# Kernel optimization log

Hardware: AMD Instinct MI355X
Metric: run time of the kernel (lower is better)

The kernel has to match this reference:

```python
import jax, jax.numpy as jnp
import numpy as np

EMBED_DIM = 1024
NUM_HEADS = 16
HEAD_DIM = EMBED_DIM // NUM_HEADS


def setup_inputs() -> dict:
    key = jax.random.key(0)
    ks = jax.random.split(key, 6)
    B, S, D = 4, 2048, EMBED_DIM
    std = 1.0 / np.sqrt(D)
    x = jax.random.normal(ks[0], (B, S, D), dtype=jnp.float32)
    wq = jax.random.normal(ks[1], (D, D), dtype=jnp.float32) * std
    wk = jax.random.normal(ks[2], (D, D), dtype=jnp.float32) * std
    wv = jax.random.normal(ks[3], (D, D), dtype=jnp.float32) * std
    wo = jax.random.normal(ks[4], (D, D), dtype=jnp.float32) * std
    bo = jax.random.normal(ks[5], (D,), dtype=jnp.float32) * 0.01
    return {"x": x, "wq": wq, "wk": wk, "wv": wv, "wo": wo, "bo": bo}


def reference(x, wq, wk, wv, wo, bo):
    B, S, D = x.shape
    H, Hd = NUM_HEADS, HEAD_DIM
    scale = 1.0 / jnp.sqrt(jnp.asarray(Hd, x.dtype))
    # nn.Linear computes x @ W.T; split into heads -> [B, H, S, Hd]
    q = (x @ wq.T).reshape(B, S, H, Hd).transpose(0, 2, 1, 3)
    k = (x @ wk.T).reshape(B, S, H, Hd).transpose(0, 2, 1, 3)
    v = (x @ wv.T).reshape(B, S, H, Hd).transpose(0, 2, 1, 3)
    scores = jnp.einsum("bhqd,bhkd->bhqk", q, k) * scale  # [B,H,S,S]
    attn = jax.nn.softmax(scores, axis=-1)
    ctx = jnp.einsum("bhqk,bhkd->bhqd", attn, v)
    ctx = ctx.transpose(0, 2, 1, 3).reshape(B, S, D)
    return ctx @ wo.T + bo
```

## Files before the change

### kernel.cpp

```cpp
#include <hip/hip_runtime.h>

typedef __bf16 bf16x8 __attribute__((ext_vector_type(8)));
typedef float f32x4 __attribute__((ext_vector_type(4)));
typedef unsigned u32x4 __attribute__((ext_vector_type(4)));
typedef unsigned short u16;

#define GAS __attribute__((address_space(1)))
#define LAS __attribute__((address_space(3)))

static __device__ __forceinline__ void gload16(const void* g, void* l) {
  __builtin_amdgcn_global_load_lds((const GAS unsigned int*)g, (LAS unsigned int*)l, 16, 0, 0);
}

static __device__ __forceinline__ u16 f2bf(float f) {
  unsigned u = __builtin_bit_cast(unsigned, f);
  u += 0x7fffu + ((u >> 16) & 1u);
  return (u16)(u >> 16);
}

static __device__ __forceinline__ unsigned pk2(float lo, float hi) {
  ushort2 u;
  u.x = __builtin_bit_cast(u16, (__bf16)lo);
  u.y = __builtin_bit_cast(u16, (__bf16)hi);
  return __builtin_bit_cast(unsigned, u);
}

__global__ void cvt_kernel(const float* __restrict__ src, u16* __restrict__ dst, int n4) {
  int i = blockIdx.x * 256 + threadIdx.x;
  if (i >= n4) return;
  float4 v = reinterpret_cast<const float4*>(src)[i];
  ushort4 o;
  o.x = f2bf(v.x); o.y = f2bf(v.y); o.z = f2bf(v.z); o.w = f2bf(v.w);
  reinterpret_cast<ushort4*>(dst)[i] = o;
}

__global__ void cvt_w_kernel(const float* __restrict__ w0, const float* __restrict__ w1,
                             const float* __restrict__ w2, const float* __restrict__ w3,
                             u16* __restrict__ d0, u16* __restrict__ d1,
                             u16* __restrict__ d2, u16* __restrict__ d3) {
  int sel = blockIdx.x >> 10;
  int i = (blockIdx.x & 1023) * 256 + threadIdx.x;
  const float* s = sel == 0 ? w0 : sel == 1 ? w1 : sel == 2 ? w2 : w3;
  u16* d = sel == 0 ? d0 : sel == 1 ? d1 : sel == 2 ? d2 : d3;
  float4 v = reinterpret_cast<const float4*>(s)[i];
  ushort4 o;
  o.x = f2bf(v.x); o.y = f2bf(v.y); o.z = f2bf(v.z); o.w = f2bf(v.w);
  reinterpret_cast<ushort4*>(d)[i] = o;
}

__global__ void gemm_qkv(const u16* __restrict__ A, const u16* __restrict__ W,
                         u16* __restrict__ Qo, u16* __restrict__ Ko, u16* __restrict__ Vo) {
  __shared__ u16 As[128 * 32];
  __shared__ u16 Bs[128 * 32];
  const int t = threadIdx.x;
  const int lane = t & 63;
  const int w = t >> 6;
  const int wr = w >> 1, wc = w & 1;
  const int l15 = lane & 15, lhi = lane >> 4;
  const int swz = (blockIdx.x & 7) * 192 + (blockIdx.x >> 3);
  const int bm = swz / 24, bn = swz % 24;

  f32x4 acc[4][4];
#pragma unroll
  for (int a = 0; a < 4; ++a)
#pragma unroll
    for (int b = 0; b < 4; ++b) acc[a][b] = (f32x4){0.f, 0.f, 0.f, 0.f};

  const u16* ag = A + (size_t)(bm * 128 + (t >> 2)) * 1024 + (t & 3) * 8;
  const u16* bg = W + (size_t)(bn * 128 + (t >> 2)) * 1024 + (t & 3) * 8;
  u16* as_p = &As[t * 8];
  u16* bs_p = &Bs[t * 8];

  for (int kt = 0; kt < 32; ++kt) {
    gload16(ag, as_p);
    gload16(ag + 64 * 1024, as_p + 2048);
    gload16(bg, bs_p);
    gload16(bg + 64 * 1024, bs_p + 2048);
    ag += 32; bg += 32;
    __syncthreads();
    bf16x8 af[4], bfr[4];
#pragma unroll
    for (int mt = 0; mt < 4; ++mt)
      af[mt] = *(const bf16x8*)&As[(wr * 64 + mt * 16 + l15) * 32 + lhi * 8];
#pragma unroll
    for (int nt = 0; nt < 4; ++nt)
      bfr[nt] = *(const bf16x8*)&Bs[(wc * 64 + nt * 16 + l15) * 32 + lhi * 8];
#pragma unroll
    for (int mt = 0; mt < 4; ++mt)
#pragma unroll
      for (int nt = 0; nt < 4; ++nt)
        acc[mt][nt] = __builtin_amdgcn_mfma_f32_16x16x32_bf16(af[mt], bfr[nt], acc[mt][nt], 0, 0, 0);
    __syncthreads();
  }

  const int tsel = bn >> 3;
  const int m0 = bm * 128 + wr * 64;
  const int n0 = bn * 128 + wc * 64;
  const int bb = bm >> 4;
  if (tsel == 0) {
    const float qs = 0.125f * 1.4426950408889634f;
#pragma unroll
    for (int nt = 0; nt < 4; ++nt) {
      int n = n0 + nt * 16 + l15;
      int c = n & 1023, h = c >> 6, hd = c & 63;
      size_t base = (size_t)(bb * 16 + h) * 2048 * 64 + hd;
#pragma unroll
      for (int mt = 0; mt < 4; ++mt)
#pragma unroll
        for (int i = 0; i < 4; ++i) {
          int s = (m0 + mt * 16 + lhi * 4 + i) & 2047;
          Qo[base + (size_t)s * 64] = f2bf(acc[mt][nt][i] * qs);
        }
    }
  } else if (tsel == 1) {
#pragma unroll
    for (int nt = 0; nt < 4; ++nt) {
      int n = n0 + nt * 16 + l15;
      int c = n & 1023, h = c >> 6, hd = c & 63;
      size_t base = (size_t)(bb * 16 + h) * 2048 * 64 + hd;
#pragma unroll
      for (int mt = 0; mt < 4; ++mt)
#pragma unroll
        for (int i = 0; i < 4; ++i) {
          int s = (m0 + mt * 16 + lhi * 4 + i) & 2047;
          Ko[base + (size_t)s * 64] = f2bf(acc[mt][nt][i]);
        }
    }
  } else {
#pragma unroll
    for (int nt = 0; nt < 4; ++nt) {
      int n = n0 + nt * 16 + l15;
      int c = n & 1023, h = c >> 6, hd = c & 63;
#pragma unroll
      for (int mt = 0; mt < 4; ++mt) {
        int s0 = (m0 + mt * 16 + lhi * 4) & 2047;
        int sp0 = ((s0 >> 4) & 1) * 4 + ((s0 >> 2) & 3) * 8 + (s0 >> 5) * 32;
        ushort4 pk;
        pk.x = f2bf(acc[mt][nt][0]);
        pk.y = f2bf(acc[mt][nt][1]);
        pk.z = f2bf(acc[mt][nt][2]);
        pk.w = f2bf(acc[mt][nt][3]);
        *(ushort4*)&Vo[((size_t)(bb * 16 + h) * 64 + hd) * 2048 + sp0] = pk;
      }
    }
  }
}

__global__ __launch_bounds__(256, 4) void attn_kernel(const u16* __restrict__ Q,
                                                      const u16* __restrict__ K,
                                                      const u16* __restrict__ Vp,
                                                      u16* __restrict__ Ctx) {
  __shared__ u16 Ks[2 * 64 * 64];
  __shared__ u16 Vs[2 * 64 * 64];
  const int t = threadIdx.x;
  const int lane = t & 63;
  const int w = t >> 6;
  const int l15 = lane & 15, lhi = lane >> 4;
  const int swz = (blockIdx.x & 7) * 128 + (blockIdx.x >> 3);
  const int qt = swz & 15, pair = swz >> 4;
  const u16* qp = Q + (size_t)pair * 2048 * 64;
  const u16* kp = K + (size_t)pair * 2048 * 64;
  const u16* vp = Vp + (size_t)pair * 64 * 2048;

  const int qrA = qt * 128 + w * 32 + l15;
  bf16x8 qfA[2], qfB[2];
  qfA[0] = *(const bf16x8*)&qp[(size_t)qrA * 64 + lhi * 8];
  qfA[1] = *(const bf16x8*)&qp[(size_t)qrA * 64 + 32 + lhi * 8];
  qfB[0] = *(const bf16x8*)&qp[(size_t)(qrA + 16) * 64 + lhi * 8];
  qfB[1] = *(const bf16x8*)&qp[(size_t)(qrA + 16) * 64 + 32 + lhi * 8];

  const u32x4 ow = {0x3F803F80u, 0x3F803F80u, 0x3F803F80u, 0x3F803F80u};
  const bf16x8 onesf = __builtin_bit_cast(bf16x8, ow);

  const int swzq = (l15 & 7) << 3;
  const int kofs0 = l15 * 64 + ((lhi * 8) ^ swzq);
  const int kofs1 = l15 * 64 + ((32 + lhi * 8) ^ swzq);

  f32x4 coA[4], coB[4], laA, laB;
  laA = (f32x4){0.f, 0.f, 0.f, 0.f};
  laB = laA;
#pragma unroll
  for (int n = 0; n < 4; ++n) { coA[n] = laA; coB[n] = laA; }

  auto stage = [&](int cb, int tt) {
#pragma unroll
    for (int j = 0; j < 2; ++j) {
      int c = j * 256 + t;
      int r = c >> 3, c8 = (c & 7) * 8;
      gload16(kp + (size_t)(tt * 64 + r) * 64 + (c8 ^ ((r & 7) << 3)), &Ks[cb + c * 8]);
    }
#pragma unroll
    for (int j = 0; j < 2; ++j) {
      int c = j * 256 + t;
      int r = c >> 3, c8 = (c & 7) * 8;
      gload16(vp + (size_t)r * 2048 + tt * 64 + (c8 ^ ((r & 7) << 3)), &Vs[cb + c * 8]);
    }
  };

  auto softmax_sub = [&](f32x4 (&sa)[4], unsigned (&pw)[4][2]) {
#pragma unroll
    for (int nt = 0; nt < 4; ++nt)
#pragma unroll
      for (int e = 0; e < 4; ++e) sa[nt][e] = __builtin_exp2f(sa[nt][e]);
#pragma unroll
    for (int nt = 0; nt < 4; ++nt) {
      pw[nt][0] = pk2(sa[nt][0], sa[nt][1]);
      pw[nt][1] = pk2(sa[nt][2], sa[nt][3]);
    }
  };

  stage(0, 0);

  for (int kt = 0; kt < 32; ++kt) {
    const int cb = (kt & 1) * 4096;
    if (kt < 31) {
      stage(cb ^ 4096, kt + 1);
      asm volatile("s_waitcnt vmcnt(4)" ::: "memory");
    } else {
      asm volatile("s_waitcnt vmcnt(0)" ::: "memory");
    }
    __builtin_amdgcn_s_barrier();

    f32x4 saA[4], saB[4];
    __builtin_amdgcn_s_setprio(1);
#pragma unroll
    for (int nt = 0; nt < 4; ++nt) {
      bf16x8 kf0 = *(const bf16x8*)&Ks[cb + kofs0 + nt * 1024];
      bf16x8 kf1 = *(const bf16x8*)&Ks[cb + kofs1 + nt * 1024];
      f32x4 zA = (f32x4){0.f, 0.f, 0.f, 0.f};
      f32x4 zB = zA;
      zA = __builtin_amdgcn_mfma_f32_16x16x32_bf16(kf0, qfA[0], zA, 0, 0, 0);
      zB = __builtin_amdgcn_mfma_f32_16x16x32_bf16(kf0, qfB[0], zB, 0, 0, 0);
      saA[nt] = __builtin_amdgcn_mfma_f32_16x16x32_bf16(kf1, qfA[1], zA, 0, 0, 0);
      saB[nt] = __builtin_amdgcn_mfma_f32_16x16x32_bf16(kf1, qfB[1], zB, 0, 0, 0);
    }
    __builtin_amdgcn_s_setprio(0);

    unsigned pwA[4][2], pwB[4][2];
    softmax_sub(saA, pwA);
    softmax_sub(saB, pwB);

    __builtin_amdgcn_s_setprio(1);
#pragma unroll
    for (int ks = 0; ks < 2; ++ks) {
      u32x4 awA = {pwA[2 * ks][0], pwA[2 * ks][1], pwA[2 * ks + 1][0], pwA[2 * ks + 1][1]};
      u32x4 awB = {pwB[2 * ks][0], pwB[2 * ks][1], pwB[2 * ks + 1][0], pwB[2 * ks + 1][1]};
      bf16x8 afA = __builtin_bit_cast(bf16x8, awA);
      bf16x8 afB = __builtin_bit_cast(bf16x8, awB);
      laA = __builtin_amdgcn_mfma_f32_16x16x32_bf16(afA, onesf, laA, 0, 0, 0);
      laB = __builtin_amdgcn_mfma_f32_16x16x32_bf16(afB, onesf, laB, 0, 0, 0);
      const int vo = l15 * 64 + (((ks ? 32 : 0) + lhi * 8) ^ swzq);
#pragma unroll
      for (int nthd = 0; nthd < 4; ++nthd) {
        bf16x8 vf = *(const bf16x8*)&Vs[cb + vo + nthd * 1024];
        coA[nthd] = __builtin_amdgcn_mfma_f32_16x16x32_bf16(afA, vf, coA[nthd], 0, 0, 0);
        coB[nthd] = __builtin_amdgcn_mfma_f32_16x16x32_bf16(afB, vf, coB[nthd], 0, 0, 0);
      }
    }
    __builtin_amdgcn_s_setprio(0);
    __builtin_amdgcn_s_barrier();
  }

  float liA[4], liB[4];
#pragma unroll
  for (int i = 0; i < 4; ++i) {
    liA[i] = 1.0f / laA[i];
    liB[i] = 1.0f / laB[i];
  }
  const int bb = pair >> 4, hh = pair & 15;
  const int sbase = qt * 128 + w * 32 + lhi * 4;
#pragma unroll
  for (int nthd = 0; nthd < 4; ++nthd) {
    int hd = nthd * 16 + l15;
#pragma unroll
    for (int i = 0; i < 4; ++i) {
      Ctx[(size_t)(bb * 2048 + sbase + i) * 1024 + hh * 64 + hd] = f2bf(coA[nthd][i] * liA[i]);
      Ctx[(size_t)(bb * 2048 + sbase + 16 + i) * 1024 + hh * 64 + hd] = f2bf(coB[nthd][i] * liB[i]);
    }
  }
}

__global__ void gemm_out(const u16* __restrict__ A, const u16* __restrict__ W,
                         const float* __restrict__ Bo, float* __restrict__ Out) {
  __shared__ u16 As[128 * 32];
  __shared__ u16 Bs[128 * 32];
  const int t = threadIdx.x;
  const int lane = t & 63;
  const int w = t >> 6;
  const int wr = w >> 1, wc = w & 1;
  const int l15 = lane & 15, lhi = lane >> 4;
  const int swz = (blockIdx.x & 7) * 64 + (blockIdx.x >> 3);
  const int bm = swz >> 3, bn = swz & 7;

  f32x4 acc[4][4];
#pragma unroll
  for (int a = 0; a < 4; ++a)
#pragma unroll
    for (int b = 0; b < 4; ++b) acc[a][b] = (f32x4){0.f, 0.f, 0.f, 0.f};

  const u16* ag = A + (size_t)(bm * 128 + (t >> 2)) * 1024 + (t & 3) * 8;
  const u16* bg = W + (size_t)(bn * 128 + (t >> 2)) * 1024 + (t & 3) * 8;
  u16* as_p = &As[t * 8];
  u16* bs_p = &Bs[t * 8];

  for (int kt = 0; kt < 32; ++kt) {
    gload16(ag, as_p);
    gload16(ag + 64 * 1024, as_p + 2048);
    gload16(bg, bs_p);
    gload16(bg + 64 * 1024, bs_p + 2048);
    ag += 32; bg += 32;
    __syncthreads();
    bf16x8 af[4], bfr[4];
#pragma unroll
    for (int mt = 0; mt < 4; ++mt)
      af[mt] = *(const bf16x8*)&As[(wr * 64 + mt * 16 + l15) * 32 + lhi * 8];
#pragma unroll
    for (int nt = 0; nt < 4; ++nt)
      bfr[nt] = *(const bf16x8*)&Bs[(wc * 64 + nt * 16 + l15) * 32 + lhi * 8];
#pragma unroll
    for (int mt = 0; mt < 4; ++mt)
#pragma unroll
      for (int nt = 0; nt < 4; ++nt)
        acc[mt][nt] = __builtin_amdgcn_mfma_f32_16x16x32_bf16(af[mt], bfr[nt], acc[mt][nt], 0, 0, 0);
    __syncthreads();
  }

  const int m0 = bm * 128 + wr * 64;
  const int n0 = bn * 128 + wc * 64;
#pragma unroll
  for (int nt = 0; nt < 4; ++nt) {
    int n = n0 + nt * 16 + l15;
    float bias = Bo[n];
#pragma unroll
    for (int mt = 0; mt < 4; ++mt)
#pragma unroll
      for (int i = 0; i < 4; ++i) {
        int m = m0 + mt * 16 + lhi * 4 + i;
        Out[(size_t)m * 1024 + n] = acc[mt][nt][i] + bias;
      }
  }
}

extern "C" void kernel_launch(void* const* d_in, const int* in_sizes, int n_in,
                              void* d_out, int out_size, void* d_ws, size_t ws_size,
                              hipStream_t stream) {
  const float* x  = (const float*)d_in[0];
  const float* wq = (const float*)d_in[1];
  const float* wk = (const float*)d_in[2];
  const float* wv = (const float*)d_in[3];
  const float* wo = (const float*)d_in[4];
  const float* bo = (const float*)d_in[5];
  float* out = (float*)d_out;

  u16* xb    = (u16*)d_ws;
  u16* wqkvb = xb + (size_t)8 * 1024 * 1024;
  u16* wob   = wqkvb + (size_t)3 * 1024 * 1024;
  u16* qb    = wob + (size_t)1 * 1024 * 1024;
  u16* kb    = qb + (size_t)8 * 1024 * 1024;
  u16* vtb   = kb + (size_t)8 * 1024 * 1024;
  u16* ctxb  = xb;

  cvt_kernel<<<8192, 256, 0, stream>>>(x, xb, 2097152);
  cvt_w_kernel<<<4096, 256, 0, stream>>>(wq, wk, wv, wo,
                                         wqkvb, wqkvb + 1048576, wqkvb + 2097152, wob);
  gemm_qkv<<<64 * 24, 256, 0, stream>>>(xb, wqkvb, qb, kb, vtb);
  attn_kernel<<<1024, 256, 0, stream>>>(qb, kb, vtb, ctxb);
  gemm_out<<<64 * 8, 256, 0, stream>>>(ctxb, wob, bo, out);
}
```

Before: 216.8 us.

## Double-buffer GEMM LDS tiles, restructure attention prefetch sync, merge conversion kernels

Both GEMM kernels now keep two LDS buffers and issue the next K-tile's global-to-LDS loads before computing on the current one. The aim is to hide global load latency behind MFMA work, and each iteration now needs only one barrier. The attention loop moves its wait and barrier to the end of the iteration, so the prefetch of the next K/V tile overlaps the whole current compute. The two fp32-to-bf16 conversion kernels become a single launch. The cost is doubled LDS per GEMM block, which may reduce occupancy.

Measured after the change: 213.4 us. Within noise of the previous version (-1.6%).

```diff
diff --git a/kernel.cpp b/kernel.cpp
--- a/kernel.cpp
+++ b/kernel.cpp
@@ -25,33 +25,36 @@
   return __builtin_bit_cast(unsigned, u);
 }
 
-__global__ void cvt_kernel(const float* __restrict__ src, u16* __restrict__ dst, int n4) {
+__global__ void cvt_all(const float* __restrict__ x, const float* __restrict__ wq,
+                        const float* __restrict__ wk, const float* __restrict__ wv,
+                        const float* __restrict__ wo, u16* __restrict__ xb,
+                        u16* __restrict__ wqkvb, u16* __restrict__ wob) {
   int i = blockIdx.x * 256 + threadIdx.x;
-  if (i >= n4) return;
-  float4 v = reinterpret_cast<const float4*>(src)[i];
+  float4 v;
+  ushort4* dst;
+  if (i < 2097152) {
+    v = reinterpret_cast<const float4*>(x)[i];
+    dst = reinterpret_cast<ushort4*>(xb) + i;
+  } else if (i < 2883584) {
+    int j = i - 2097152;
+    const float* s = j < 262144 ? wq : (j < 524288 ? wk : wv);
+    int jj = j < 262144 ? j : (j < 524288 ? j - 262144 : j - 524288);
+    v = reinterpret_cast<const float4*>(s)[jj];
+    dst = reinterpret_cast<ushort4*>(wqkvb) + j;
+  } else {
+    int j = i - 2883584;
+    v = reinterpret_cast<const float4*>(wo)[j];
+    dst = reinterpret_cast<ushort4*>(wob) + j;
+  }
   ushort4 o;
   o.x = f2bf(v.x); o.y = f2bf(v.y); o.z = f2bf(v.z); o.w = f2bf(v.w);
-  reinterpret_cast<ushort4*>(dst)[i] = o;
-}
-
-__global__ void cvt_w_kernel(const float* __restrict__ w0, const float* __restrict__ w1,
-                             const float* __restrict__ w2, const float* __restrict__ w3,
-                             u16* __restrict__ d0, u16* __restrict__ d1,
-                             u16* __restrict__ d2, u16* __restrict__ d3) {
-  int sel = blockIdx.x >> 10;
-  int i = (blockIdx.x & 1023) * 256 + threadIdx.x;
-  const float* s = sel == 0 ? w0 : sel == 1 ? w1 : sel == 2 ? w2 : w3;
-  u16* d = sel == 0 ? d0 : sel == 1 ? d1 : sel == 2 ? d2 : d3;
-  float4 v = reinterpret_cast<const float4*>(s)[i];
-  ushort4 o;
-  o.x = f2bf(v.x); o.y = f2bf(v.y); o.z = f2bf(v.z); o.w = f2bf(v.w);
-  reinterpret_cast<ushort4*>(d)[i] = o;
+  *dst = o;
 }
 
 __global__ void gemm_qkv(const u16* __restrict__ A, const u16* __restrict__ W,
                          u16* __restrict__ Qo, u16* __restrict__ Ko, u16* __restrict__ Vo) {
-  __shared__ u16 As[128 * 32];
-  __shared__ u16 Bs[128 * 32];
+  __shared__ u16 As[2 * 128 * 32];
+  __shared__ u16 Bs[2 * 128 * 32];
   const int t = threadIdx.x;
   const int lane = t & 63;
   const int w = t >> 6;
@@ -68,29 +71,35 @@
 
   const u16* ag = A + (size_t)(bm * 128 + (t >> 2)) * 1024 + (t & 3) * 8;
   const u16* bg = W + (size_t)(bn * 128 + (t >> 2)) * 1024 + (t & 3) * 8;
-  u16* as_p = &As[t * 8];
-  u16* bs_p = &Bs[t * 8];
+
+  auto stage = [&](int cb, int kt) {
+    gload16(ag + kt * 32, &As[cb + t * 8]);
+    gload16(ag + kt * 32 + 64 * 1024, &As[cb + t * 8 + 2048]);
+    gload16(bg + kt * 32, &Bs[cb + t * 8]);
+    gload16(bg + kt * 32 + 64 * 1024, &Bs[cb + t * 8 + 2048]);
+  };
+
+  stage(0, 0);
+  asm volatile("s_waitcnt vmcnt(0)" ::: "memory");
+  __builtin_amdgcn_s_barrier();
 
   for (int kt = 0; kt < 32; ++kt) {
-    gload16(ag, as_p);
-    gload16(ag + 64 * 1024, as_p + 2048);
-    gload16(bg, bs_p);
-    gload16(bg + 64 * 1024, bs_p + 2048);
-    ag += 32; bg += 32;
-    __syncthreads();
+    const int cb = (kt & 1) * 4096;
+    if (kt < 31) stage(cb ^ 4096, kt + 1);
     bf16x8 af[4], bfr[4];
 #pragma unroll
     for (int mt = 0; mt < 4; ++mt)
-      af[mt] = *(const bf16x8*)&As[(wr * 64 + mt * 16 + l15) * 32 + lhi * 8];
+      af[mt] = *(const bf16x8*)&As[cb + (wr * 64 + mt * 16 + l15) * 32 + lhi * 8];
 #pragma unroll
     for (int nt = 0; nt < 4; ++nt)
-      bfr[nt] = *(const bf16x8*)&Bs[(wc * 64 + nt * 16 + l15) * 32 + lhi * 8];
+      bfr[nt] = *(const bf16x8*)&Bs[cb + (wc * 64 + nt * 16 + l15) * 32 + lhi * 8];
 #pragma unroll
     for (int mt = 0; mt < 4; ++mt)
 #pragma unroll
       for (int nt = 0; nt < 4; ++nt)
         acc[mt][nt] = __builtin_amdgcn_mfma_f32_16x16x32_bf16(af[mt], bfr[nt], acc[mt][nt], 0, 0, 0);
-    __syncthreads();
+    asm volatile("s_waitcnt vmcnt(0)" ::: "memory");
+    __builtin_amdgcn_s_barrier();
   }
 
   const int tsel = bn >> 3;
@@ -175,6 +184,8 @@
   const int swzq = (l15 & 7) << 3;
   const int kofs0 = l15 * 64 + ((lhi * 8) ^ swzq);
   const int kofs1 = l15 * 64 + ((32 + lhi * 8) ^ swzq);
+  const int vofs0 = l15 * 64 + ((lhi * 8) ^ swzq);
+  const int vofs1 = l15 * 64 + ((32 + lhi * 8) ^ swzq);
 
   f32x4 coA[4], coB[4], laA, laB;
   laA = (f32x4){0.f, 0.f, 0.f, 0.f};
@@ -210,16 +221,12 @@
   };
 
   stage(0, 0);
+  asm volatile("s_waitcnt vmcnt(0)" ::: "memory");
+  __builtin_amdgcn_s_barrier();
 
   for (int kt = 0; kt < 32; ++kt) {
     const int cb = (kt & 1) * 4096;
-    if (kt < 31) {
-      stage(cb ^ 4096, kt + 1);
-      asm volatile("s_waitcnt vmcnt(4)" ::: "memory");
-    } else {
-      asm volatile("s_waitcnt vmcnt(0)" ::: "memory");
-    }
-    __builtin_amdgcn_s_barrier();
+    if (kt < 31) stage(cb ^ 4096, kt + 1);
 
     f32x4 saA[4], saB[4];
     __builtin_amdgcn_s_setprio(1);
@@ -249,7 +256,7 @@
       bf16x8 afB = __builtin_bit_cast(bf16x8, awB);
       laA = __builtin_amdgcn_mfma_f32_16x16x32_bf16(afA, onesf, laA, 0, 0, 0);
       laB = __builtin_amdgcn_mfma_f32_16x16x32_bf16(afB, onesf, laB, 0, 0, 0);
-      const int vo = l15 * 64 + (((ks ? 32 : 0) + lhi * 8) ^ swzq);
+      const int vo = ks ? vofs1 : vofs0;
 #pragma unroll
       for (int nthd = 0; nthd < 4; ++nthd) {
         bf16x8 vf = *(const bf16x8*)&Vs[cb + vo + nthd * 1024];
@@ -258,6 +265,8 @@
       }
     }
     __builtin_amdgcn_s_setprio(0);
+
+    asm volatile("s_waitcnt vmcnt(0)" ::: "memory");
     __builtin_amdgcn_s_barrier();
   }
 
@@ -282,8 +291,8 @@
 
 __global__ void gemm_out(const u16* __restrict__ A, const u16* __restrict__ W,
                          const float* __restrict__ Bo, float* __restrict__ Out) {
-  __shared__ u16 As[128 * 32];
-  __shared__ u16 Bs[128 * 32];
+  __shared__ u16 As[2 * 128 * 32];
+  __shared__ u16 Bs[2 * 128 * 32];
   const int t = threadIdx.x;
   const int lane = t & 63;
   const int w = t >> 6;
@@ -300,29 +309,35 @@
 
   const u16* ag = A + (size_t)(bm * 128 + (t >> 2)) * 1024 + (t & 3) * 8;
   const u16* bg = W + (size_t)(bn * 128 + (t >> 2)) * 1024 + (t & 3) * 8;
-  u16* as_p = &As[t * 8];
-  u16* bs_p = &Bs[t * 8];
+
+  auto stage = [&](int cb, int kt) {
+    gload16(ag + kt * 32, &As[cb + t * 8]);
+    gload16(ag + kt * 32 + 64 * 1024, &As[cb + t * 8 + 2048]);
+    gload16(bg + kt * 32, &Bs[cb + t * 8]);
+    gload16(bg + kt * 32 + 64 * 1024, &Bs[cb + t * 8 + 2048]);
+  };
+
+  stage(0, 0);
+  asm volatile("s_waitcnt vmcnt(0)" ::: "memory");
+  __builtin_amdgcn_s_barrier();
 
   for (int kt = 0; kt < 32; ++kt) {
-    gload16(ag, as_p);
-    gload16(ag + 64 * 1024, as_p + 2048);
-    gload16(bg, bs_p);
-    gload16(bg + 64 * 1024, bs_p + 2048);
-    ag += 32; bg += 32;
-    __syncthreads();
+    const int cb = (kt & 1) * 4096;
+    if (kt < 31) stage(cb ^ 4096, kt + 1);
     bf16x8 af[4], bfr[4];
 #pragma unroll
     for (int mt = 0; mt < 4; ++mt)
-      af[mt] = *(const bf16x8*)&As[(wr * 64 + mt * 16 + l15) * 32 + lhi * 8];
+      af[mt] = *(const bf16x8*)&As[cb + (wr * 64 + mt * 16 + l15) * 32 + lhi * 8];
 #pragma unroll
     for (int nt = 0; nt < 4; ++nt)
-      bfr[nt] = *(const bf16x8*)&Bs[(wc * 64 + nt * 16 + l15) * 32 + lhi * 8];
+      bfr[nt] = *(const bf16x8*)&Bs[cb + (wc * 64 + nt * 16 + l15) * 32 + lhi * 8];
 #pragma unroll
     for (int mt = 0; mt < 4; ++mt)
 #pragma unroll
       for (int nt = 0; nt < 4; ++nt)
         acc[mt][nt] = __builtin_amdgcn_mfma_f32_16x16x32_bf16(af[mt], bfr[nt], acc[mt][nt], 0, 0, 0);
-    __syncthreads();
+    asm volatile("s_waitcnt vmcnt(0)" ::: "memory");
+    __builtin_amdgcn_s_barrier();
   }
 
   const int m0 = bm * 128 + wr * 64;
@@ -360,9 +375,7 @@
   u16* vtb   = kb + (size_t)8 * 1024 * 1024;
   u16* ctxb  = xb;
 
-  cvt_kernel<<<8192, 256, 0, stream>>>(x, xb, 2097152);
-  cvt_w_kernel<<<4096, 256, 0, stream>>>(wq, wk, wv, wo,
-                                         wqkvb, wqkvb + 1048576, wqkvb + 2097152, wob);
+  cvt_all<<<12288, 256, 0, stream>>>(x, wq, wk, wv, wo, xb, wqkvb, wob);
   gemm_qkv<<<64 * 24, 256, 0, stream>>>(xb, wqkvb, qb, kb, vtb);
   attn_kernel<<<1024, 256, 0, stream>>>(qb, kb, vtb, ctxb);
   gemm_out<<<64 * 8, 256, 0, stream>>>(ctxb, wob, bo, out);
```
